# Kernel tuning notes

Hardware: AMD Instinct MI355X
Metric: run time of the kernel (lower is better)

## Reference

```python
import jax, jax.numpy as jnp
import numpy as np

NN = 128  # number of neighbors (self.nn in the torch module)


def _safe_cdist(A, B):
    # Euclidean pairwise distance with grad-safe sqrt at exact zeros
    sq = (jnp.sum(A * A, -1)[..., :, None]
          + jnp.sum(B * B, -1)[..., None, :]
          - 2.0 * jnp.matmul(A, jnp.swapaxes(B, -1, -2)))
    sq = jnp.maximum(sq, 0.0)
    pos = sq > 0
    return jnp.where(pos, jnp.sqrt(jnp.where(pos, sq, 1.0)), 0.0)


def _kernel(A, B, lv, av):
    # a * exp(-cdist(A/l, B/l) / sqrt(D))
    d = _safe_cdist(A / lv, B / lv) / np.sqrt(A.shape[-1])
    return av * jnp.exp(-d)


def setup_inputs() -> dict:
    key = jax.random.key(0)
    k = jax.random.split(key, 5)
    B, N, D, O = 1024, 100000, 256, 1
    return {
        "x": jax.random.normal(k[0], (B, D), jnp.float32),
        "trainX": jax.random.normal(k[1], (N, D), jnp.float32),
        "trainy": jax.random.normal(k[2], (N, O), jnp.float32),
        "noise": jax.random.normal(k[3], (B, NN, O), jnp.float32),
        "l": jnp.zeros((), jnp.float32),
        "a": jnp.zeros((), jnp.float32),
        "ymean": jnp.zeros((), jnp.float32),
    }


def reference(x, trainX, trainy, noise, l, a, ymean):
    lv = jnp.exp(l)
    av = jnp.exp(a)
    # [B, N] distances, kNN retrieval (eval path: topk of nn, no self-exclusion)
    dists = _safe_cdist(x / lv, trainX / lv)
    _, neighbors = jax.lax.top_k(-dists, NN)          # smallest distances
    nX = trainX[neighbors]                            # [B, NN, D]
    ny = trainy[neighbors] + 0.01 * noise - ymean     # [B, NN, O]
    auto = _kernel(nX, nX, lv, av)                    # [B, NN, NN]
    autoCov = jnp.linalg.inv(auto)                    # batched 128x128 inverse
    crossCov = _kernel(x[:, None, :], nX, lv, av)     # [B, 1, NN]
    kW = crossCov @ autoCov                           # [B, 1, NN]
    y = kW @ ny                                       # [B, 1, O]
    yVar = av * jnp.ones(x.shape[0], x.dtype) - jnp.squeeze(
        kW @ jnp.swapaxes(crossCov, -1, -2))          # [B]
    return (jnp.squeeze(y + ymean, 1), yVar)
```

## Files before the change

### kernel.cpp

```cpp
#include <hip/hip_runtime.h>
#include <math.h>
#include <stdint.h>

#define B_SZ    1024
#define N_TRAIN 100000
#define N_PAD   100096
#define D_DIM   256
#define NN      128
#define KSEL    256
#define CAP     2048
#define NSAMP   1024
#define SRANK   8

typedef unsigned short u16;
typedef unsigned long long u64;
typedef __attribute__((ext_vector_type(8))) short short8v;
typedef __attribute__((ext_vector_type(4))) float f32x4;

__device__ inline u16 f2bf(float f) {
    unsigned u = __float_as_uint(f);
    return (u16)((u + 0x7FFFu + ((u >> 16) & 1u)) >> 16);
}
__device__ inline float bf2f(u16 h) { return __uint_as_float((unsigned)h << 16); }

__global__ __launch_bounds__(256) void kprep(const float* __restrict__ trainX,
                                             const float* __restrict__ x,
                                             float* __restrict__ tt,
                                             float* __restrict__ xx,
                                             u16* __restrict__ Bh,
                                             u16* __restrict__ Bl,
                                             u16* __restrict__ Ah) {
    int wave = (blockIdx.x * blockDim.x + threadIdx.x) >> 6;
    int lane = threadIdx.x & 63;
    if (wave >= N_TRAIN + B_SZ) return;
    const bool isTrain = wave < N_TRAIN;
    const float* row = isTrain ? (trainX + (size_t)wave * D_DIM)
                               : (x + (size_t)(wave - N_TRAIN) * D_DIM);
    float4 v = ((const float4*)row)[lane];
    float s = v.x*v.x + v.y*v.y + v.z*v.z + v.w*v.w;
    for (int off = 32; off; off >>= 1) s += __shfl_down(s, off, 64);
    u16 h0 = f2bf(v.x), h1 = f2bf(v.y), h2 = f2bf(v.z), h3 = f2bf(v.w);
    u64 hp = (u64)h0 | ((u64)h1 << 16) | ((u64)h2 << 32) | ((u64)h3 << 48);
    if (isTrain) {
        ((u64*)(Bh + (size_t)wave * D_DIM))[lane] = hp;
        u16 l0 = f2bf(v.x - bf2f(h0)), l1 = f2bf(v.y - bf2f(h1));
        u16 l2 = f2bf(v.z - bf2f(h2)), l3 = f2bf(v.w - bf2f(h3));
        ((u64*)(Bl + (size_t)wave * D_DIM))[lane] =
            (u64)l0 | ((u64)l1 << 16) | ((u64)l2 << 32) | ((u64)l3 << 48);
        if (lane == 0) tt[wave] = s;
    } else {
        ((u64*)(Ah + (size_t)(wave - N_TRAIN) * D_DIM))[lane] = hp;
        if (lane == 0) xx[wave - N_TRAIN] = s;
    }
}

__global__ __launch_bounds__(256) void k1m(const u16* __restrict__ Ah,
                                           const u16* __restrict__ Bh,
                                           const float* __restrict__ xx,
                                           const float* __restrict__ tt,
                                           u16* __restrict__ distu,
                                           int row0, int nrows) {
    __shared__ u16 Als[4][128][8];
    __shared__ u16 Bls[4][128][8];
    const int tid = threadIdx.x;
    const int lane = tid & 63, wv = tid >> 6;
    const int wr = wv >> 1, wc = wv & 1;
    const int ib = blockIdx.y * 128;
    const size_t jb = (size_t)blockIdx.x * 128;

    f32x4 acc[4][4];
    #pragma unroll
    for (int m = 0; m < 4; ++m)
        #pragma unroll
        for (int n = 0; n < 4; ++n)
            #pragma unroll
            for (int r = 0; r < 4; ++r) acc[m][n][r] = 0.f;

    for (int k0 = 0; k0 < D_DIM; k0 += 32) {
        #pragma unroll
        for (int r = 0; r < 2; ++r) {
            int c = tid + r * 256;
            int row = c >> 2, ks = c & 3;
            uint4 va = make_uint4(0, 0, 0, 0);
            if (ib + row < nrows)
                va = *(const uint4*)(Ah + (size_t)(row0 + ib + row) * D_DIM + k0 + ks * 8);
            *(uint4*)(&Als[ks][row][0]) = va;
            uint4 vb = make_uint4(0, 0, 0, 0);
            if (jb + row < N_TRAIN)
                vb = *(const uint4*)(Bh + (jb + row) * D_DIM + k0 + ks * 8);
            *(uint4*)(&Bls[ks][row][0]) = vb;
        }
        __syncthreads();
        const int ksl = lane >> 4, li = lane & 15;
        short8v a[4], b[4];
        #pragma unroll
        for (int m = 0; m < 4; ++m)
            a[m] = *(const short8v*)&Als[ksl][wr * 64 + m * 16 + li][0];
        #pragma unroll
        for (int n = 0; n < 4; ++n)
            b[n] = *(const short8v*)&Bls[ksl][wc * 64 + n * 16 + li][0];
        #pragma unroll
        for (int m = 0; m < 4; ++m)
            #pragma unroll
            for (int n = 0; n < 4; ++n)
                acc[m][n] = __builtin_amdgcn_mfma_f32_16x16x32_bf16(a[m], b[n], acc[m][n], 0, 0, 0);
        __syncthreads();
    }
    const int li = lane & 15, lh = lane >> 4;
    float ttv[4]; int cols[4];
    #pragma unroll
    for (int n = 0; n < 4; ++n) {
        cols[n] = (int)jb + wc * 64 + n * 16 + li;
        ttv[n] = (cols[n] < N_TRAIN) ? tt[cols[n]] : 0.f;
    }
    #pragma unroll
    for (int m = 0; m < 4; ++m)
        #pragma unroll
        for (int r = 0; r < 4; ++r) {
            int rl = ib + wr * 64 + m * 16 + lh * 4 + r;
            if (rl >= nrows) continue;
            float xi = xx[row0 + rl];
            u64 pk = 0;
            #pragma unroll
            for (int n = 0; n < 4; ++n) {
                u16 code = 0xFFFFu;
                if (cols[n] < N_TRAIN)
                    code = f2bf(fmaxf(xi + ttv[n] - 2.0f * acc[m][n][r], 0.f));
                pk |= (u64)code << (16 * n);
            }
            *(u64*)(distu + (size_t)rl * N_PAD + jb + wc * 64 + li * 4) = pk;
        }
}

__device__ inline void bitonicU64N(u64* a, int tid, int NE) {
    for (int ks = 2; ks <= NE; ks <<= 1)
        for (int js = ks >> 1; js > 0; js >>= 1) {
            __syncthreads();
            for (int e = tid; e < NE; e += 256) {
                int p = e ^ js;
                if (p > e) {
                    u64 A = a[e], B = a[p];
                    if ((A > B) == ((e & ks) == 0)) { a[e] = B; a[p] = A; }
                }
            }
        }
    __syncthreads();
}
__device__ inline void bitonicU16N(u16* a, int tid, int NE) {
    for (int ks = 2; ks <= NE; ks <<= 1)
        for (int js = ks >> 1; js > 0; js >>= 1) {
            __syncthreads();
            for (int e = tid; e < NE; e += 256) {
                int p = e ^ js;
                if (p > e) {
                    u16 A = a[e], B = a[p];
                    if ((A > B) == ((e & ks) == 0)) { a[e] = B; a[p] = A; }
                }
            }
        }
    __syncthreads();
}

__global__ __launch_bounds__(256) void k2_select(const u16* __restrict__ distu, int row0,
                                                 const float* __restrict__ x,
                                                 const float* __restrict__ trainX,
                                                 const float* __restrict__ xx,
                                                 const float* __restrict__ tt,
                                                 int* __restrict__ nidx,
                                                 float* __restrict__ nsq) {
    const int tid = threadIdx.x;
    const int b = row0 + blockIdx.x;
    const u16* row = distu + (size_t)blockIdx.x * N_PAD;
    const uint4* row8 = (const uint4*)row;
    __shared__ u64 buf[CAP];
    __shared__ int s_cnt;
    __shared__ int sIdx[KSEL];
    __shared__ float4 xs4[64];
    u16* samp = (u16*)buf;

    if (tid < NSAMP / 8) ((uint4*)samp)[tid] = row8[tid];
    __syncthreads();
    bitonicU16N(samp, tid, NSAMP);
    int Tc = (int)samp[SRANK];
    __syncthreads();

    int cnt = 0;
    for (int att = 0; att < 8; ++att) {
        if (tid == 0) s_cnt = 0;
        __syncthreads();
        for (int j8 = tid; j8 < N_PAD / 8; j8 += 256) {
            uint4 v = row8[j8];
            unsigned w_[4] = {v.x, v.y, v.z, v.w};
            #pragma unroll
            for (int c2 = 0; c2 < 4; ++c2) {
                #pragma unroll
                for (int hc = 0; hc < 2; ++hc) {
                    int code = (int)(hc ? (w_[c2] >> 16) : (w_[c2] & 0xFFFFu));
                    if (code < Tc) {
                        int p = atomicAdd(&s_cnt, 1);
                        if (p < CAP) buf[p] = ((u64)(unsigned)code << 32)
                                            | (unsigned)(j8 * 8 + c2 * 2 + hc);
                    }
                }
            }
        }
        __syncthreads();
        cnt = s_cnt;
        if (cnt >= KSEL && cnt <= CAP) break;
        Tc += (cnt < KSEL) ? 8 : -8;
        __syncthreads();
    }
    if (cnt > CAP) cnt = CAP;
    int NE = KSEL;
    while (NE < cnt) NE <<= 1;
    for (int i = tid; i < NE; i += 256) if (i >= cnt) buf[i] = ~0ull;
    __syncthreads();
    bitonicU64N(buf, tid, NE);
    {
        u64 e = buf[tid];
        int jraw = (e == ~0ull) ? 0 : (int)(e & 0xFFFFFFFFull);
        int base = (jraw >> 7) << 7, off = jraw & 127;
        sIdx[tid] = base + (off & 64) + ((off & 3) << 4) + ((off & 63) >> 2);
    }
    if (tid < 64) xs4[tid] = ((const float4*)(x + (size_t)b * D_DIM))[tid];
    __syncthreads();

    const int lane = tid & 63, wv = tid >> 6;
    const int ls = lane & 31;
    const float xxb = xx[b];
    for (int it = 0; it < KSEL / 8; ++it) {
        int c = it * 8 + wv * 2 + (lane >> 5);
        int j = sIdx[c];
        const float4* tr = (const float4*)(trainX + (size_t)j * D_DIM);
        float4 p1 = tr[ls * 2], p2 = tr[ls * 2 + 1];
        float4 q1 = xs4[ls * 2], q2 = xs4[ls * 2 + 1];
        float d = p1.x*q1.x + p1.y*q1.y + p1.z*q1.z + p1.w*q1.w
                + p2.x*q2.x + p2.y*q2.y + p2.z*q2.z + p2.w*q2.w;
        #pragma unroll
        for (int m = 1; m < 32; m <<= 1) d += __shfl_xor(d, m, 64);
        if (ls == 0) {
            float sq = fmaxf(xxb + tt[j] - 2.0f * d, 0.f);
            buf[c] = ((u64)__float_as_uint(sq) << 32) | (unsigned)j;
        }
    }
    __syncthreads();
    bitonicU64N(buf, tid, KSEL);
    if (tid < NN) {
        u64 e = buf[tid];
        nidx[(size_t)b * NN + tid] = (int)(e & 0xFFFFFFFFull);
        nsq[(size_t)b * NN + tid]  = __uint_as_float((unsigned)(e >> 32));
    }
}

__global__ __launch_bounds__(256, 2) void k3_solve(
    const u16* __restrict__ Bh, const u16* __restrict__ Bl,
    const float* __restrict__ trainy,
    const float* __restrict__ noise, const float* __restrict__ tt,
    const int* __restrict__ nidx, const float* __restrict__ nsq,
    const float* __restrict__ lp, const float* __restrict__ ap,
    const float* __restrict__ ymp, float* __restrict__ out) {

    __shared__ u16 Shi[128][40];
    __shared__ u16 Slo[128][40];
    __shared__ __align__(16) float pbufT[2][NN][4];
    __shared__ float diagb[2][4][4];
    __shared__ float yLds[NN], yfwd[NN], dvec[NN], wvec[NN];
    __shared__ int   idxs[NN];
    __shared__ float ttn[NN], c0v[NN];
    __shared__ float red[8];

    const int b = blockIdx.x;
    const int tid = threadIdx.x;
    const int lane = tid & 63, wv = tid >> 6;
    const int wr = wv >> 1, wc = wv & 1;
    const int lr = lane & 15, lq = lane >> 4;

    const float lv = expf(lp[0]);
    const float av = expf(ap[0]);
    const float ymean = ymp[0];
    const float sc = 1.0f / (lv * 16.0f);

    if (tid < NN) {
        int ix = nidx[(size_t)b * NN + tid];
        idxs[tid] = ix;
        ttn[tid] = tt[ix];
        float cc = av * expf(-sqrtf(nsq[(size_t)b * NN + tid]) * sc);
        c0v[tid] = cc;
        yLds[tid] = cc;
    }
    __syncthreads();

    f32x4 acc[4][4];
    #pragma unroll
    for (int m = 0; m < 4; ++m)
        #pragma unroll
        for (int n = 0; n < 4; ++n)
            #pragma unroll
            for (int r = 0; r < 4; ++r) acc[m][n][r] = 0.f;

    for (int c = 0; c < 8; ++c) {
        #pragma unroll
        for (int s = 0; s < 2; ++s) {
            int idx = tid + s * 256;
            int row = idx >> 2, kp = (idx & 3) << 3;
            size_t base = (size_t)idxs[row] * D_DIM + c * 32 + kp;
            *(uint4*)&Shi[row][kp] = *(const uint4*)(Bh + base);
            *(uint4*)&Slo[row][kp] = *(const uint4*)(Bl + base);
        }
        __syncthreads();
        {
            short8v ahi[4], bhi[4];
            #pragma unroll
            for (int m = 0; m < 4; ++m)
                ahi[m] = *(const short8v*)&Shi[wr * 64 + m * 16 + lr][lq * 8];
            #pragma unroll
            for (int n = 0; n < 4; ++n)
                bhi[n] = *(const short8v*)&Shi[wc * 64 + n * 16 + lr][lq * 8];
            #pragma unroll
            for (int m = 0; m < 4; ++m)
                #pragma unroll
                for (int n = 0; n < 4; ++n)
                    acc[m][n] = __builtin_amdgcn_mfma_f32_16x16x32_bf16(ahi[m], bhi[n], acc[m][n], 0, 0, 0);
            #pragma unroll
            for (int n = 0; n < 4; ++n) {
                short8v blo = *(const short8v*)&Slo[wc * 64 + n * 16 + lr][lq * 8];
                #pragma unroll
                for (int m = 0; m < 4; ++m)
                    acc[m][n] = __builtin_amdgcn_mfma_f32_16x16x32_bf16(ahi[m], blo, acc[m][n], 0, 0, 0);
            }
            #pragma unroll
            for (int m = 0; m < 4; ++m) {
                short8v alo = *(const short8v*)&Slo[wr * 64 + m * 16 + lr][lq * 8];
                #pragma unroll
                for (int n = 0; n < 4; ++n)
                    acc[m][n] = __builtin_amdgcn_mfma_f32_16x16x32_bf16(alo, bhi[n], acc[m][n], 0, 0, 0);
            }
        }
        __syncthreads();
    }

    float em[4][4][4];
    #pragma unroll
    for (int m = 0; m < 4; ++m) {
        #pragma unroll
        for (int r = 0; r < 4; ++r) {
            int i = wr * 64 + m * 16 + lq * 4 + r;
            float ti = ttn[i];
            #pragma unroll
            for (int n = 0; n < 4; ++n) {
                int j = wc * 64 + n * 16 + lr;
                float sq = fmaxf(ti + ttn[j] - 2.0f * acc[m][n][r], 0.0f);
                em[m][n][r] = av * expf(-sqrtf(sq) * sc);
            }
        }
    }

    for (int kb = 0; kb < 32; ++kb) {
        const int k0 = kb * 4;
        const int par = kb & 1;
        if (wr == (k0 >> 6) && lq == ((k0 & 15) >> 2)) {
            #pragma unroll
            for (int mm = 0; mm < 4; ++mm)
                if (mm == ((k0 >> 4) & 3)) {
                    #pragma unroll
                    for (int n = 0; n < 4; ++n) {
                        int j = wc * 64 + n * 16 + lr;
                        *(float4*)&pbufT[par][j][0] =
                            make_float4(em[mm][n][0], em[mm][n][1], em[mm][n][2], em[mm][n][3]);
                        int cd = j - k0;
                        if (cd >= 0 && cd < 4) {
                            #pragma unroll
                            for (int r = 0; r < 4; ++r)
                                diagb[par][r][cd] = em[mm][n][r];
                        }
                    }
                }
        }
        __syncthreads();
        float d0 = diagb[par][0][0], i0 = 1.0f / d0;
        float B01 = diagb[par][0][1], B02 = diagb[par][0][2], B03 = diagb[par][0][3];
        float l10 = diagb[par][1][0] * i0;
        float l20 = diagb[par][2][0] * i0;
        float l30 = diagb[par][3][0] * i0;
        float d1 = diagb[par][1][1] - l10 * B01, i1 = 1.0f / d1;
        float t12 = diagb[par][1][2] - l10 * B02;
        float t13 = diagb[par][1][3] - l10 * B03;
        float l21 = (diagb[par][2][1] - l20 * B01) * i1;
        float l31 = (diagb[par][3][1] - l30 * B01) * i1;
        float d2 = diagb[par][2][2] - l20 * B02 - l21 * t12, i2 = 1.0f / d2;
        float t23 = diagb[par][2][3] - l20 * B03 - l21 * t13;
        float l32 = (diagb[par][3][2] - l30 * B02 - l31 * t12) * i2;
        float d3 = diagb[par][3][3] - l30 * B03 - l31 * t13 - l32 * t23, i3 = 1.0f / d3;
        if (tid < 128) {
            float4 a = *(const float4*)&pbufT[par][tid][0];
            float a1 = a.y - l10 * a.x;
            float a2 = a.z - l20 * a.x - l21 * a1;
            float a3 = a.w - l30 * a.x - l31 * a1 - l32 * a2;
            a.y = a1; a.z = a2; a.w = a3;
            *(float4*)&pbufT[par][tid][0] = a;
        }
        __syncthreads();
        float cj0[4], cj1[4], cj2[4], cj3[4];
        #pragma unroll
        for (int n = 0; n < 4; ++n) {
            int j = wc * 64 + n * 16 + lr;
            float4 cv = *(const float4*)&pbufT[par][j][0];
            cj0[n] = (j > k0)     ? cv.x : 0.f;
            cj1[n] = (j > k0 + 1) ? cv.y : 0.f;
            cj2[n] = (j > k0 + 2) ? cv.z : 0.f;
            cj3[n] = (j > k0 + 3) ? cv.w : 0.f;
        }
        #pragma unroll
        for (int m = 0; m < 4; ++m)
            #pragma unroll
            for (int rr = 0; rr < 4; ++rr) {
                int i = wr * 64 + m * 16 + lq * 4 + rr;
                float4 rv = *(const float4*)&pbufT[par][i][0];
                float k0v = (i > k0)     ? rv.x * i0 : 0.f;
                float k1v = (i > k0 + 1) ? rv.y * i1 : 0.f;
                float k2v = (i > k0 + 2) ? rv.z * i2 : 0.f;
                float k3v = (i > k0 + 3) ? rv.w * i3 : 0.f;
                #pragma unroll
                for (int n = 0; n < 4; ++n) {
                    float t = em[m][n][rr];
                    t = fmaf(-k0v, cj0[n], t);
                    t = fmaf(-k1v, cj1[n], t);
                    t = fmaf(-k2v, cj2[n], t);
                    t = fmaf(-k3v, cj3[n], t);
                    em[m][n][rr] = t;
                }
            }
        if (wc == 0 && lr == 0) {
            float fy0 = yLds[k0];
            float fy1 = yLds[k0+1] - l10 * fy0;
            float fy2 = yLds[k0+2] - l20 * fy0 - l21 * fy1;
            float fy3 = yLds[k0+3] - l30 * fy0 - l31 * fy1 - l32 * fy2;
            #pragma unroll
            for (int m = 0; m < 4; ++m)
                #pragma unroll
                for (int rr = 0; rr < 4; ++rr) {
                    int i = wr * 64 + m * 16 + lq * 4 + rr;
                    if (i > k0 + 3) {
                        float4 rv = *(const float4*)&pbufT[par][i][0];
                        float yv = yLds[i];
                        yv = fmaf(-rv.x * i0, fy0, yv);
                        yv = fmaf(-rv.y * i1, fy1, yv);
                        yv = fmaf(-rv.z * i2, fy2, yv);
                        yv = fmaf(-rv.w * i3, fy3, yv);
                        yLds[i] = yv;
                    }
                }
            if (tid == 0) {
                dvec[k0] = d0; dvec[k0+1] = d1; dvec[k0+2] = d2; dvec[k0+3] = d3;
                yfwd[k0] = fy0; yfwd[k0+1] = fy1; yfwd[k0+2] = fy2; yfwd[k0+3] = fy3;
            }
        }
    }
    __syncthreads();
    if (tid < NN) yLds[tid] = yfwd[tid];
    __syncthreads();

    for (int kb = 31; kb >= 0; --kb) {
        const int k0 = kb * 4;
        const int par = kb & 1;
        {
            int q = lr - (k0 & 15);
            if (wc == (k0 >> 6) && q >= 0 && q < 4) {
                #pragma unroll
                for (int nn = 0; nn < 4; ++nn)
                    if (nn == ((k0 >> 4) & 3)) {
                        #pragma unroll
                        for (int m = 0; m < 4; ++m)
                            #pragma unroll
                            for (int r = 0; r < 4; ++r)
                                pbufT[par][wr * 64 + m * 16 + lq * 4 + r][q] = em[m][nn][r];
                    }
            }
        }
        __syncthreads();
        float w3 = yLds[k0+3] / dvec[k0+3];
        float w2 = (yLds[k0+2] - pbufT[par][k0+2][3] * w3) / dvec[k0+2];
        float w1 = (yLds[k0+1] - pbufT[par][k0+1][2] * w2 - pbufT[par][k0+1][3] * w3) / dvec[k0+1];
        float w0 = (yLds[k0]   - pbufT[par][k0][1] * w1 - pbufT[par][k0][2] * w2
                               - pbufT[par][k0][3] * w3) / dvec[k0];
        if (tid == 0) { wvec[k0] = w0; wvec[k0+1] = w1; wvec[k0+2] = w2; wvec[k0+3] = w3; }
        if (tid < k0) {
            float4 pv = *(const float4*)&pbufT[par][tid][0];
            float yv = yLds[tid];
            yv = fmaf(-pv.x, w0, yv);
            yv = fmaf(-pv.y, w1, yv);
            yv = fmaf(-pv.z, w2, yv);
            yv = fmaf(-pv.w, w3, yv);
            yLds[tid] = yv;
        }
    }
    __syncthreads();

    float p1 = 0.f, p2 = 0.f;
    if (tid < NN) {
        float w = wvec[tid];
        float nyv = trainy[idxs[tid]] + 0.01f * noise[(size_t)b * NN + tid] - ymean;
        p1 = w * nyv;
        p2 = w * c0v[tid];
    }
    for (int off = 32; off; off >>= 1) {
        p1 += __shfl_down(p1, off, 64);
        p2 += __shfl_down(p2, off, 64);
    }
    if ((tid & 63) == 0) { red[wv * 2] = p1; red[wv * 2 + 1] = p2; }
    __syncthreads();
    if (tid == 0) {
        out[b]        = (red[0] + red[2] + red[4] + red[6]) + ymean;
        out[B_SZ + b] = av - (red[1] + red[3] + red[5] + red[7]);
    }
}

extern "C" void kernel_launch(void* const* d_in, const int* in_sizes, int n_in,
                              void* d_out, int out_size, void* d_ws, size_t ws_size,
                              hipStream_t stream) {
    const float* x      = (const float*)d_in[0];
    const float* trainX = (const float*)d_in[1];
    const float* trainy = (const float*)d_in[2];
    const float* noise  = (const float*)d_in[3];
    const float* lp     = (const float*)d_in[4];
    const float* ap     = (const float*)d_in[5];
    const float* ymp    = (const float*)d_in[6];
    float* out = (float*)d_out;

    char* ws = (char*)d_ws;
    size_t off = 0;
    auto alloc = [&](size_t bytes) {
        void* p = ws + off;
        off = (off + bytes + 255) & ~(size_t)255;
        return p;
    };
    float* tt   = (float*)alloc((size_t)N_TRAIN * 4);
    float* xx   = (float*)alloc((size_t)B_SZ * 4);
    int*   nidb = (int*)  alloc((size_t)B_SZ * NN * 4);
    float* nsqb = (float*)alloc((size_t)B_SZ * NN * 4);
    u16*   Ah   = (u16*)  alloc((size_t)B_SZ * D_DIM * 2);
    u16*   Bh   = (u16*)  alloc((size_t)N_TRAIN * D_DIM * 2);
    u16*   Bl   = (u16*)  alloc((size_t)N_TRAIN * D_DIM * 2);
    size_t distBytes = (ws_size > off) ? (ws_size - off) : 0;
    u16* distu = (u16*)(ws + off);
    int R = (int)(distBytes / ((size_t)N_PAD * 2));
    if (R > B_SZ) R = B_SZ;
    if (R < 1) R = 1;

    {
        int waves = N_TRAIN + B_SZ;
        kprep<<<(waves + 3) / 4, 256, 0, stream>>>(trainX, x, tt, xx, Bh, Bl, Ah);
    }

    for (int r0 = 0; r0 < B_SZ; r0 += R) {
        int rc = (B_SZ - r0 < R) ? (B_SZ - r0) : R;
        dim3 g1((N_TRAIN + 127) / 128, (rc + 127) / 128);
        k1m<<<g1, 256, 0, stream>>>(Ah, Bh, xx, tt, distu, r0, rc);
        k2_select<<<rc, 256, 0, stream>>>(distu, r0, x, trainX, xx, tt, nidb, nsqb);
    }
    k3_solve<<<B_SZ, 256, 0, stream>>>(Bh, Bl, trainy, noise, tt, nidb, nsqb,
                                       lp, ap, ymp, out);
}
```

Before: 627.8 us.

## Remove a barrier per Cholesky panel step and prefetch the next panel into the alternate buffer

In the blocked LDL forward elimination, the separate panel triangular-solve pass and its __syncthreads are removed. Each thread now recomputes the panel's forward substitution on the fly from the raw panel values it loads. The next panel (and, in back substitution, the next column block) is published to the double buffer right after the current update, so each step needs one barrier instead of two. This adds redundant per-thread arithmetic and relies on the parity double buffering to avoid read/write races.

```diff
diff --git a/kernel.cpp b/kernel.cpp
--- a/kernel.cpp
+++ b/kernel.cpp
@@ -355,27 +355,49 @@
         }
     }
 
+    auto publishPanel = [&](int kb2) {
+        const int k0p = kb2 * 4;
+        const int parp = kb2 & 1;
+        if (wr == (k0p >> 6) && lq == ((k0p & 15) >> 2)) {
+            #pragma unroll
+            for (int mm = 0; mm < 4; ++mm)
+                if (mm == ((k0p >> 4) & 3)) {
+                    #pragma unroll
+                    for (int n = 0; n < 4; ++n) {
+                        int j = wc * 64 + n * 16 + lr;
+                        *(float4*)&pbufT[parp][j][0] =
+                            make_float4(em[mm][n][0], em[mm][n][1], em[mm][n][2], em[mm][n][3]);
+                        int cd = j - k0p;
+                        if (cd >= 0 && cd < 4) {
+                            #pragma unroll
+                            for (int r = 0; r < 4; ++r)
+                                diagb[parp][r][cd] = em[mm][n][r];
+                        }
+                    }
+                }
+        }
+    };
+    auto publishCols = [&](int kb2) {
+        const int k0p = kb2 * 4;
+        const int parp = kb2 & 1;
+        int q = lr - (k0p & 15);
+        if (wc == (k0p >> 6) && q >= 0 && q < 4) {
+            #pragma unroll
+            for (int nn = 0; nn < 4; ++nn)
+                if (nn == ((k0p >> 4) & 3)) {
+                    #pragma unroll
+                    for (int m = 0; m < 4; ++m)
+                        #pragma unroll
+                        for (int r = 0; r < 4; ++r)
+                            pbufT[parp][wr * 64 + m * 16 + lq * 4 + r][q] = em[m][nn][r];
+                }
+        }
+    };
+
+    publishPanel(0);
     for (int kb = 0; kb < 32; ++kb) {
         const int k0 = kb * 4;
         const int par = kb & 1;
-        if (wr == (k0 >> 6) && lq == ((k0 & 15) >> 2)) {
-            #pragma unroll
-            for (int mm = 0; mm < 4; ++mm)
-                if (mm == ((k0 >> 4) & 3)) {
-                    #pragma unroll
-                    for (int n = 0; n < 4; ++n) {
-                        int j = wc * 64 + n * 16 + lr;
-                        *(float4*)&pbufT[par][j][0] =
-                            make_float4(em[mm][n][0], em[mm][n][1], em[mm][n][2], em[mm][n][3]);
-                        int cd = j - k0;
-                        if (cd >= 0 && cd < 4) {
-                            #pragma unroll
-                            for (int r = 0; r < 4; ++r)
-                                diagb[par][r][cd] = em[mm][n][r];
-                        }
-                    }
-                }
-        }
         __syncthreads();
         float d0 = diagb[par][0][0], i0 = 1.0f / d0;
         float B01 = diagb[par][0][1], B02 = diagb[par][0][2], B03 = diagb[par][0][3];
@@ -391,24 +413,19 @@
         float t23 = diagb[par][2][3] - l20 * B03 - l21 * t13;
         float l32 = (diagb[par][3][2] - l30 * B02 - l31 * t12) * i2;
         float d3 = diagb[par][3][3] - l30 * B03 - l31 * t13 - l32 * t23, i3 = 1.0f / d3;
-        if (tid < 128) {
-            float4 a = *(const float4*)&pbufT[par][tid][0];
-            float a1 = a.y - l10 * a.x;
-            float a2 = a.z - l20 * a.x - l21 * a1;
-            float a3 = a.w - l30 * a.x - l31 * a1 - l32 * a2;
-            a.y = a1; a.z = a2; a.w = a3;
-            *(float4*)&pbufT[par][tid][0] = a;
-        }
-        __syncthreads();
         float cj0[4], cj1[4], cj2[4], cj3[4];
         #pragma unroll
         for (int n = 0; n < 4; ++n) {
             int j = wc * 64 + n * 16 + lr;
             float4 cv = *(const float4*)&pbufT[par][j][0];
-            cj0[n] = (j > k0)     ? cv.x : 0.f;
-            cj1[n] = (j > k0 + 1) ? cv.y : 0.f;
-            cj2[n] = (j > k0 + 2) ? cv.z : 0.f;
-            cj3[n] = (j > k0 + 3) ? cv.w : 0.f;
+            float a0 = cv.x;
+            float a1 = cv.y - l10 * a0;
+            float a2 = cv.z - l20 * a0 - l21 * a1;
+            float a3 = cv.w - l30 * a0 - l31 * a1 - l32 * a2;
+            cj0[n] = (j > k0)     ? a0 : 0.f;
+            cj1[n] = (j > k0 + 1) ? a1 : 0.f;
+            cj2[n] = (j > k0 + 2) ? a2 : 0.f;
+            cj3[n] = (j > k0 + 3) ? a3 : 0.f;
         }
         #pragma unroll
         for (int m = 0; m < 4; ++m)
@@ -416,10 +433,14 @@
             for (int rr = 0; rr < 4; ++rr) {
                 int i = wr * 64 + m * 16 + lq * 4 + rr;
                 float4 rv = *(const float4*)&pbufT[par][i][0];
-                float k0v = (i > k0)     ? rv.x * i0 : 0.f;
-                float k1v = (i > k0 + 1) ? rv.y * i1 : 0.f;
-                float k2v = (i > k0 + 2) ? rv.z * i2 : 0.f;
-                float k3v = (i > k0 + 3) ? rv.w * i3 : 0.f;
+                float b0 = rv.x;
+                float b1 = rv.y - l10 * b0;
+                float b2 = rv.z - l20 * b0 - l21 * b1;
+                float b3 = rv.w - l30 * b0 - l31 * b1 - l32 * b2;
+                float k0v = (i > k0)     ? b0 * i0 : 0.f;
+                float k1v = (i > k0 + 1) ? b1 * i1 : 0.f;
+                float k2v = (i > k0 + 2) ? b2 * i2 : 0.f;
+                float k3v = (i > k0 + 3) ? b3 * i3 : 0.f;
                 #pragma unroll
                 for (int n = 0; n < 4; ++n) {
                     float t = em[m][n][rr];
@@ -442,11 +463,15 @@
                     int i = wr * 64 + m * 16 + lq * 4 + rr;
                     if (i > k0 + 3) {
                         float4 rv = *(const float4*)&pbufT[par][i][0];
+                        float b0 = rv.x;
+                        float b1 = rv.y - l10 * b0;
+                        float b2 = rv.z - l20 * b0 - l21 * b1;
+                        float b3 = rv.w - l30 * b0 - l31 * b1 - l32 * b2;
                         float yv = yLds[i];
-                        yv = fmaf(-rv.x * i0, fy0, yv);
-                        yv = fmaf(-rv.y * i1, fy1, yv);
-                        yv = fmaf(-rv.z * i2, fy2, yv);
-                        yv = fmaf(-rv.w * i3, fy3, yv);
+                        yv = fmaf(-b0 * i0, fy0, yv);
+                        yv = fmaf(-b1 * i1, fy1, yv);
+                        yv = fmaf(-b2 * i2, fy2, yv);
+                        yv = fmaf(-b3 * i3, fy3, yv);
                         yLds[i] = yv;
                     }
                 }
@@ -455,29 +480,18 @@
                 yfwd[k0] = fy0; yfwd[k0+1] = fy1; yfwd[k0+2] = fy2; yfwd[k0+3] = fy3;
             }
         }
+        if (kb < 31) publishPanel(kb + 1);
     }
     __syncthreads();
     if (tid < NN) yLds[tid] = yfwd[tid];
     __syncthreads();
 
+    publishCols(31);
     for (int kb = 31; kb >= 0; --kb) {
         const int k0 = kb * 4;
         const int par = kb & 1;
-        {
-            int q = lr - (k0 & 15);
-            if (wc == (k0 >> 6) && q >= 0 && q < 4) {
-                #pragma unroll
-                for (int nn = 0; nn < 4; ++nn)
-                    if (nn == ((k0 >> 4) & 3)) {
-                        #pragma unroll
-                        for (int m = 0; m < 4; ++m)
-                            #pragma unroll
-                            for (int r = 0; r < 4; ++r)
-                                pbufT[par][wr * 64 + m * 16 + lq * 4 + r][q] = em[m][nn][r];
-                    }
-            }
-        }
-        __syncthreads();
+        __syncthreads();
+        if (kb > 0) publishCols(kb - 1);
         float w3 = yLds[k0+3] / dvec[k0+3];
         float w2 = (yLds[k0+2] - pbufT[par][k0+2][3] * w3) / dvec[k0+2];
         float w1 = (yLds[k0+1] - pbufT[par][k0+1][2] * w2 - pbufT[par][k0+1][3] * w3) / dvec[k0+1];
```

After: 798.7 us. 1.27x slower.

## Split neighbor-kernel solve into separate Gram-build and solve kernels

Applied to the files above, without the earlier changes.

The fused k3_solve kernel is split in two. k3a builds the 128x128 kernel matrix with MFMA and writes the exponentiated entries to a global workspace (16 MB). k3b reads them back and runs the sequential inverse/solve. This lets each phase use its own launch bounds and register budget for higher occupancy, at the cost of a global round trip and an extra launch.

```diff
diff --git a/kernel.cpp b/kernel.cpp
--- a/kernel.cpp
+++ b/kernel.cpp
@@ -252,22 +252,16 @@
     }
 }
 
-__global__ __launch_bounds__(256, 2) void k3_solve(
+__global__ __launch_bounds__(256, 4) void k3a(
     const u16* __restrict__ Bh, const u16* __restrict__ Bl,
-    const float* __restrict__ trainy,
-    const float* __restrict__ noise, const float* __restrict__ tt,
-    const int* __restrict__ nidx, const float* __restrict__ nsq,
+    const float* __restrict__ tt, const int* __restrict__ nidx,
     const float* __restrict__ lp, const float* __restrict__ ap,
-    const float* __restrict__ ymp, float* __restrict__ out) {
+    float4* __restrict__ emG) {
 
     __shared__ u16 Shi[128][40];
     __shared__ u16 Slo[128][40];
-    __shared__ __align__(16) float pbufT[2][NN][4];
-    __shared__ float diagb[2][4][4];
-    __shared__ float yLds[NN], yfwd[NN], dvec[NN], wvec[NN];
     __shared__ int   idxs[NN];
-    __shared__ float ttn[NN], c0v[NN];
-    __shared__ float red[8];
+    __shared__ float ttn[NN];
 
     const int b = blockIdx.x;
     const int tid = threadIdx.x;
@@ -277,16 +271,12 @@
 
     const float lv = expf(lp[0]);
     const float av = expf(ap[0]);
-    const float ymean = ymp[0];
     const float sc = 1.0f / (lv * 16.0f);
 
     if (tid < NN) {
         int ix = nidx[(size_t)b * NN + tid];
         idxs[tid] = ix;
         ttn[tid] = tt[ix];
-        float cc = av * expf(-sqrtf(nsq[(size_t)b * NN + tid]) * sc);
-        c0v[tid] = cc;
-        yLds[tid] = cc;
     }
     __syncthreads();
 
@@ -339,21 +329,68 @@
         __syncthreads();
     }
 
+    #pragma unroll
+    for (int m = 0; m < 4; ++m)
+        #pragma unroll
+        for (int n = 0; n < 4; ++n) {
+            int j = wc * 64 + n * 16 + lr;
+            float tj = ttn[j];
+            float4 o;
+            #pragma unroll
+            for (int r = 0; r < 4; ++r) {
+                int i = wr * 64 + m * 16 + lq * 4 + r;
+                float sq = fmaxf(ttn[i] + tj - 2.0f * acc[m][n][r], 0.0f);
+                float val = av * expf(-sqrtf(sq) * sc);
+                if (r == 0) o.x = val; else if (r == 1) o.y = val;
+                else if (r == 2) o.z = val; else o.w = val;
+            }
+            emG[((size_t)b * 16 + (m * 4 + n)) * 256 + tid] = o;
+        }
+}
+
+__global__ __launch_bounds__(256, 3) void k3b(
+    const float4* __restrict__ emG,
+    const float* __restrict__ trainy, const float* __restrict__ noise,
+    const int* __restrict__ nidx, const float* __restrict__ nsq,
+    const float* __restrict__ lp, const float* __restrict__ ap,
+    const float* __restrict__ ymp, float* __restrict__ out) {
+
+    __shared__ __align__(16) float pbufT[2][NN][4];
+    __shared__ float diagb[2][4][4];
+    __shared__ float yLds[NN], yfwd[NN], dvec[NN], wvec[NN];
+    __shared__ int   idxs[NN];
+    __shared__ float c0v[NN];
+    __shared__ float red[8];
+
+    const int b = blockIdx.x;
+    const int tid = threadIdx.x;
+    const int lane = tid & 63, wv = tid >> 6;
+    const int wr = wv >> 1, wc = wv & 1;
+    const int lr = lane & 15, lq = lane >> 4;
+
+    const float lv = expf(lp[0]);
+    const float av = expf(ap[0]);
+    const float ymean = ymp[0];
+    const float sc = 1.0f / (lv * 16.0f);
+
+    if (tid < NN) {
+        int ix = nidx[(size_t)b * NN + tid];
+        idxs[tid] = ix;
+        float cc = av * expf(-sqrtf(nsq[(size_t)b * NN + tid]) * sc);
+        c0v[tid] = cc;
+        yLds[tid] = cc;
+    }
+
     float em[4][4][4];
     #pragma unroll
-    for (int m = 0; m < 4; ++m) {
-        #pragma unroll
-        for (int r = 0; r < 4; ++r) {
-            int i = wr * 64 + m * 16 + lq * 4 + r;
-            float ti = ttn[i];
-            #pragma unroll
-            for (int n = 0; n < 4; ++n) {
-                int j = wc * 64 + n * 16 + lr;
-                float sq = fmaxf(ti + ttn[j] - 2.0f * acc[m][n][r], 0.0f);
-                em[m][n][r] = av * expf(-sqrtf(sq) * sc);
-            }
-        }
-    }
+    for (int q = 0; q < 16; ++q) {
+        float4 v = emG[((size_t)b * 16 + q) * 256 + tid];
+        em[q >> 2][q & 3][0] = v.x;
+        em[q >> 2][q & 3][1] = v.y;
+        em[q >> 2][q & 3][2] = v.z;
+        em[q >> 2][q & 3][3] = v.w;
+    }
+    __syncthreads();
 
     for (int kb = 0; kb < 32; ++kb) {
         const int k0 = kb * 4;
@@ -541,6 +578,7 @@
     u16*   Ah   = (u16*)  alloc((size_t)B_SZ * D_DIM * 2);
     u16*   Bh   = (u16*)  alloc((size_t)N_TRAIN * D_DIM * 2);
     u16*   Bl   = (u16*)  alloc((size_t)N_TRAIN * D_DIM * 2);
+    float4* emG = (float4*)alloc((size_t)B_SZ * 16 * 256 * 16);
     size_t distBytes = (ws_size > off) ? (ws_size - off) : 0;
     u16* distu = (u16*)(ws + off);
     int R = (int)(distBytes / ((size_t)N_PAD * 2));
@@ -558,6 +596,6 @@
         k1m<<<g1, 256, 0, stream>>>(Ah, Bh, xx, tt, distu, r0, rc);
         k2_select<<<rc, 256, 0, stream>>>(distu, r0, x, trainX, xx, tt, nidb, nsqb);
     }
-    k3_solve<<<B_SZ, 256, 0, stream>>>(Bh, Bl, trainy, noise, tt, nidb, nsqb,
-                                       lp, ap, ymp, out);
-}
+    k3a<<<B_SZ, 256, 0, stream>>>(Bh, Bl, tt, nidb, lp, ap, emG);
+    k3b<<<B_SZ, 256, 0, stream>>>(emG, trainy, noise, nidb, nsqb, lp, ap, ymp, out);
+}
```

Result: slower. 1.393 ms (+121.9%).
